# Optimization experiments

Hardware: AMD Instinct MI355X
Metric: run time of the kernel (lower is better)

## Reference

```python
import jax, jax.numpy as jnp
import numpy as np

WS = 7            # window size
NW = 64           # windows per image ((56/7)^2)
SHIFT = 3         # shift size for the SW-MSA mask
HW = 56           # spatial patch grid


def _build_rel_index():
    coords = np.stack(np.meshgrid(np.arange(WS), np.arange(WS), indexing='ij'))  # [2,7,7]
    flat = coords.reshape(2, -1)                                                 # [2,49]
    rel = (flat[:, :, None] - flat[:, None, :]).transpose(1, 2, 0)               # [49,49,2]
    rel[:, :, 0] += WS - 1
    rel[:, :, 1] += WS - 1
    rel[:, :, 0] *= 2 * WS - 1
    return rel.sum(-1).astype(np.int32)                                          # [49,49]


def _build_shift_mask():
    img = np.zeros((HW, HW), dtype=np.float32)
    cnt = 0
    sl = (slice(0, -WS), slice(-WS, -SHIFT), slice(-SHIFT, None))
    for h in sl:
        for w in sl:
            img[h, w] = cnt
            cnt += 1
    # window partition -> [nW, 49]
    mw = img.reshape(HW // WS, WS, HW // WS, WS).transpose(0, 2, 1, 3).reshape(-1, WS * WS)
    am = mw[:, None, :] - mw[:, :, None]                                          # [nW,49,49]
    return np.where(am != 0, -100.0, 0.0).astype(np.float32)


def setup_inputs() -> dict:
    key = jax.random.key(0)
    ks = jax.random.split(key, 6)
    dim, heads, N = 128, 4, WS * WS
    B_ = 4096
    return {
        'x': jax.random.normal(ks[0], (B_, N, dim), dtype=jnp.float32),
        'qkv_w': jax.random.normal(ks[1], (dim, 3 * dim), dtype=jnp.float32) * 0.02,
        'qkv_b': jax.random.normal(ks[2], (3 * dim,), dtype=jnp.float32) * 0.02,
        'proj_w': jax.random.normal(ks[3], (dim, dim), dtype=jnp.float32) * 0.02,
        'proj_b': jax.random.normal(ks[4], (dim,), dtype=jnp.float32) * 0.02,
        'rel_bias_table': jax.random.normal(ks[5], ((2 * WS - 1) ** 2, heads), dtype=jnp.float32) * 0.02,
        'mask': jnp.asarray(_build_shift_mask()),
        'rel_index': jnp.asarray(_build_rel_index()),
    }


def reference(x, qkv_w, qkv_b, proj_w, proj_b, rel_bias_table, mask, rel_index):
    B_, N, C = x.shape
    heads = rel_bias_table.shape[1]
    hd = C // heads
    scale = hd ** -0.5
    # fused qkv projection: [B_, N, 3, H, hd]
    qkv = (x @ qkv_w + qkv_b).reshape(B_, N, 3, heads, hd)
    q, k, v = qkv[:, :, 0], qkv[:, :, 1], qkv[:, :, 2]      # [B_, N, H, hd]
    attn = jnp.einsum('bnhd,bmhd->bhnm', q, k) * scale       # [B_, H, N, N]
    # relative position bias gather: [N,N,H] -> [H,N,N]
    bias = rel_bias_table[rel_index].transpose(2, 0, 1)
    attn = attn + bias[None]
    # shifted-window mask: mask [nW, N, N]
    nW = mask.shape[0]
    attn = attn.reshape(B_ // nW, nW, heads, N, N) + mask[None, :, None]
    attn = attn.reshape(B_, heads, N, N)
    attn = jax.nn.softmax(attn, axis=-1)
    out = jnp.einsum('bhnm,bmhd->bnhd', attn, v).reshape(B_, N, C)
    return out @ proj_w + proj_b
```

## Files before the change

kernel.cpp:

```cpp
#include <hip/hip_runtime.h>
#include <hip/hip_bf16.h>

typedef __attribute__((ext_vector_type(8))) short bf16x8;
typedef __attribute__((ext_vector_type(4))) short s16x4;
typedef __attribute__((ext_vector_type(4))) float f32x4;

#define NTOK 49

#define XROW    136
#define RVB     8704
#define VBT_STR 68
#define VBT_SZ  2176
#define RQK     17408
#define QK_SZ   3920
#define SM_TOT  33088

__device__ __forceinline__ short f2b(float v) {
    __hip_bfloat16 b = __float2bfloat16(v);
    return *reinterpret_cast<short*>(&b);
}

__device__ __forceinline__ int rid_of(int t, int wh, int ww) {
    int i = t / 7;
    int j = t - 7 * i;
    int rh = (wh == 7) ? ((i < 4) ? 1 : 2) : 0;
    int rw = (ww == 7) ? ((j < 4) ? 1 : 2) : 0;
    return rh * 3 + rw;
}

__global__ void prep_kernel(const float* __restrict__ qkv_w,
                            const float* __restrict__ proj_w,
                            const float* __restrict__ rel_tab,
                            const int*   __restrict__ rel_idx,
                            short* __restrict__ wqkv_t,
                            short* __restrict__ wproj_t,
                            float* __restrict__ bmp2) {
    int i = blockIdx.x * 256 + threadIdx.x;
    if (i < 384 * 128) {
        int n = i >> 7, k = i & 127;
        wqkv_t[i] = f2b(qkv_w[k * 384 + n]);
        return;
    }
    int j = i - 384 * 128;
    if (j < 128 * 128) {
        int n = j >> 7, k = j & 127;
        wproj_t[j] = f2b(proj_w[k * 128 + n]);
        return;
    }
    int l = j - 128 * 128;
    if (l < 16 * NTOK * 64) {
        const float LOG2E = 1.4426950408889634f;
        int wt  = l / (4 * NTOK * 64);
        int rem = l - wt * (4 * NTOK * 64);
        int h   = rem / (NTOK * 64);
        int rm2 = rem - h * (NTOK * 64);
        int q = rm2 >> 6, kk = rm2 & 63;
        float v;
        if (kk < NTOK) {
            v = rel_tab[rel_idx[q * NTOK + kk] * 4 + h] * LOG2E;
            int wh = (wt & 1) ? 7 : 0, ww = (wt & 2) ? 7 : 0;
            if (rid_of(q, wh, ww) != rid_of(kk, wh, ww)) v -= 100.0f * LOG2E;
        } else {
            v = -1e30f;
        }
        bmp2[l] = v;
    }
}

__launch_bounds__(512, 4)
__global__ void swin_fused(const float* __restrict__ x,
                           const short* __restrict__ wqkv_t,
                           const float* __restrict__ qkv_b,
                           const short* __restrict__ wproj_t,
                           const float* __restrict__ proj_b,
                           const float* __restrict__ bmp2,
                           float* __restrict__ out) {
    __shared__ short sm[SM_TOT];

    const int b   = blockIdx.x;
    const int tid = threadIdx.x;
    const int wv  = tid >> 6;
    const int ln  = tid & 63;
    const int g   = ln >> 4;
    const int c   = ln & 15;
    const int h    = wv >> 1;
    const int half = wv & 1;

    short* vbt = sm + RVB + h * VBT_SZ;
    short* qbh = sm + RQK + h * QK_SZ;
    short* kbh = qbh + 1960;
    short* pbh = qbh;

    const int cq = 32 * h + 16 * half;

    if (tid < 510) {
        *(s16x4*)&sm[NTOK * XROW + tid * 4] = (s16x4){0, 0, 0, 0};
    }
    for (int idx = tid; idx < 128 * 15; idx += 512) {
        int d = idx / 15, t = 49 + (idx - (idx / 15) * 15);
        sm[RVB + (d >> 5) * VBT_SZ + (d & 31) * VBT_STR + t] = 0;
    }
    {
        const f32x4* xp4 = (const f32x4*)(x + (size_t)b * 6272);
        f32x4 v0 = xp4[tid];
        f32x4 v1 = xp4[tid + 512];
        f32x4 v2 = xp4[tid + 1024];
        f32x4 v3;
        if (tid < 32) v3 = xp4[tid + 1536];
        #define XWR(IDX, V) { int row = (IDX) >> 5; int col = ((IDX) & 31) * 4; \
            s16x4 pk; pk[0]=f2b((V)[0]); pk[1]=f2b((V)[1]); pk[2]=f2b((V)[2]); pk[3]=f2b((V)[3]); \
            *(s16x4*)&sm[row * XROW + col] = pk; }
        XWR(tid, v0) XWR(tid + 512, v1) XWR(tid + 1024, v2)
        if (tid < 32) XWR(tid + 1536, v3)
        #undef XWR
    }
    bf16x8 wqr[4], wkr[4];
    #pragma unroll
    for (int kt = 0; kt < 4; ++kt) {
        wqr[kt] = *(const bf16x8*)&wqkv_t[(cq + c) * 128 + 32*kt + 8*g];
        wkr[kt] = *(const bf16x8*)&wqkv_t[(128 + cq + c) * 128 + 32*kt + 8*g];
    }
    __syncthreads();

    bf16x8 wvr[4];
    {
        f32x4 accq[4], acck[4];
        #pragma unroll
        for (int nt = 0; nt < 4; ++nt) { accq[nt] = (f32x4){0.f,0.f,0.f,0.f}; acck[nt] = (f32x4){0.f,0.f,0.f,0.f}; }
        #pragma unroll
        for (int kt = 0; kt < 4; ++kt) {
            bf16x8 xv[4];
            #pragma unroll
            for (int nt = 0; nt < 4; ++nt)
                xv[nt] = *(const bf16x8*)&sm[(16*nt + c) * XROW + 32*kt + 8*g];
            #pragma unroll
            for (int nt = 0; nt < 4; ++nt) {
                accq[nt] = __builtin_amdgcn_mfma_f32_16x16x32_bf16(wqr[kt], xv[nt], accq[nt], 0, 0, 0);
                acck[nt] = __builtin_amdgcn_mfma_f32_16x16x32_bf16(wkr[kt], xv[nt], acck[nt], 0, 0, 0);
            }
        }
        #pragma unroll
        for (int kt = 0; kt < 4; ++kt)
            wvr[kt] = *(const bf16x8*)&wqkv_t[(256 + cq + c) * 128 + 32*kt + 8*g];

        const float qsc = 0.17677669529663687f * 1.4426950408889634f;
        f32x4 bq4 = *(const f32x4*)&qkv_b[cq + 4*g];
        f32x4 bk4 = *(const f32x4*)&qkv_b[128 + cq + 4*g];
        #pragma unroll
        for (int nt = 0; nt < 4; ++nt) {
            int tok = 16*nt + c;
            if (tok >= NTOK) continue;
            s16x4 pq, pk2;
            #pragma unroll
            for (int r = 0; r < 4; ++r) {
                pq[r]  = f2b((accq[nt][r] + bq4[r]) * qsc);
                pk2[r] = f2b(acck[nt][r] + bk4[r]);
            }
            *(s16x4*)&qbh[tok * 40 + 16*half + 4*g] = pq;
            *(s16x4*)&kbh[tok * 40 + 16*half + 4*g] = pk2;
        }
    }

    {
        f32x4 accv[4];
        #pragma unroll
        for (int nt = 0; nt < 4; ++nt) accv[nt] = (f32x4){0.f,0.f,0.f,0.f};
        #pragma unroll
        for (int kt = 0; kt < 4; ++kt) {
            bf16x8 xv[4];
            #pragma unroll
            for (int nt = 0; nt < 4; ++nt)
                xv[nt] = *(const bf16x8*)&sm[(16*nt + c) * XROW + 32*kt + 8*g];
            #pragma unroll
            for (int nt = 0; nt < 4; ++nt)
                accv[nt] = __builtin_amdgcn_mfma_f32_16x16x32_bf16(wvr[kt], xv[nt], accv[nt], 0, 0, 0);
        }
        f32x4 bv4 = *(const f32x4*)&qkv_b[256 + cq + 4*g];
        const int d0 = 16*half + 4*g;
        #pragma unroll
        for (int nt = 0; nt < 4; ++nt) {
            int tok = 16*nt + c;
            if (tok >= NTOK) continue;
            vbt[(d0+0) * VBT_STR + tok] = f2b(accv[nt][0] + bv4[0]);
            vbt[(d0+1) * VBT_STR + tok] = f2b(accv[nt][1] + bv4[1]);
            vbt[(d0+2) * VBT_STR + tok] = f2b(accv[nt][2] + bv4[2]);
            vbt[(d0+3) * VBT_STR + tok] = f2b(accv[nt][3] + bv4[3]);
        }
    }

    const int ntq0 = 2 * half;
    const int wt = ((((b >> 3) & 7) == 7) ? 1 : 0) | (((b & 7) == 7) ? 2 : 0);
    const float* bbase = bmp2 + ((size_t)(wt * 4 + h) * NTOK) * 64;
    f32x4 bias0[4], bias1[4];
    {
        int q0c = 16*ntq0 + c;       if (q0c > 48) q0c = 48;
        int q1c = 16*(ntq0+1) + c;   if (q1c > 48) q1c = 48;
        const float* bp0 = bbase + (size_t)q0c * 64;
        const float* bp1 = bbase + (size_t)q1c * 64;
        #pragma unroll
        for (int mt = 0; mt < 4; ++mt) {
            bias0[mt] = *(const f32x4*)&bp0[16*mt + 4*g];
            bias1[mt] = *(const f32x4*)&bp1[16*mt + 4*g];
        }
    }
    __syncthreads();

    f32x4 sA[4][2];
    {
        #pragma unroll
        for (int mt = 0; mt < 4; ++mt) { sA[mt][0] = (f32x4){0.f,0.f,0.f,0.f}; sA[mt][1] = (f32x4){0.f,0.f,0.f,0.f}; }
        bf16x8 ak[4];
        #pragma unroll
        for (int mt = 0; mt < 4; ++mt) {
            int kt2 = 16*mt + c; if (kt2 > 48) kt2 = 48;
            ak[mt] = *(const bf16x8*)&kbh[kt2 * 40 + 8*g];
        }
        #pragma unroll
        for (int jj = 0; jj < 2; ++jj) {
            int qt = 16*(ntq0+jj) + c; if (qt > 48) qt = 48;
            bf16x8 bq = *(const bf16x8*)&qbh[qt * 40 + 8*g];
            #pragma unroll
            for (int mt = 0; mt < 4; ++mt)
                sA[mt][jj] = __builtin_amdgcn_mfma_f32_16x16x32_bf16(ak[mt], bq, sA[mt][jj], 0, 0, 0);
        }
    }
    __syncthreads();

    {
        float rs01[2];
        #pragma unroll
        for (int jj = 0; jj < 2; ++jj) {
            int qtok = 16*(ntq0+jj) + c;
            const f32x4* bias = jj ? bias1 : bias0;
            float e[16];
            float mx = -1e30f;
            #pragma unroll
            for (int mt = 0; mt < 4; ++mt) {
                #pragma unroll
                for (int r = 0; r < 4; ++r) {
                    float v = sA[mt][jj][r] + bias[mt][r];
                    e[4*mt+r] = v;
                    mx = fmaxf(mx, v);
                }
            }
            mx = fmaxf(mx, __shfl_xor(mx, 16, 64));
            mx = fmaxf(mx, __shfl_xor(mx, 32, 64));
            float s = 0.f;
            #pragma unroll
            for (int ii = 0; ii < 16; ++ii) { float ev = exp2f(e[ii] - mx); e[ii] = ev; s += ev; }
            if (qtok < NTOK) {
                #pragma unroll
                for (int mt = 0; mt < 4; ++mt) {
                    s16x4 pk;
                    pk[0] = f2b(e[4*mt+0]);
                    pk[1] = f2b(e[4*mt+1]);
                    pk[2] = f2b(e[4*mt+2]);
                    pk[3] = f2b(e[4*mt+3]);
                    *(s16x4*)&pbh[qtok * 72 + 16*mt + 4*g] = pk;
                }
            }
            s += __shfl_xor(s, 16, 64);
            s += __shfl_xor(s, 32, 64);
            rs01[jj] = 1.0f / s;
        }

        f32x4 o[2][2];
        o[0][0]=(f32x4){0.f,0.f,0.f,0.f}; o[0][1]=(f32x4){0.f,0.f,0.f,0.f};
        o[1][0]=(f32x4){0.f,0.f,0.f,0.f}; o[1][1]=(f32x4){0.f,0.f,0.f,0.f};
        #pragma unroll
        for (int kt = 0; kt < 2; ++kt) {
            bf16x8 av[2];
            #pragma unroll
            for (int mt = 0; mt < 2; ++mt)
                av[mt] = *(const bf16x8*)&vbt[(16*mt + c) * VBT_STR + 32*kt + 8*g];
            #pragma unroll
            for (int jj = 0; jj < 2; ++jj) {
                int qt = 16*(ntq0+jj) + c; if (qt > 48) qt = 48;
                bf16x8 bp2 = *(const bf16x8*)&pbh[qt * 72 + 32*kt + 8*g];
                #pragma unroll
                for (int mt = 0; mt < 2; ++mt)
                    o[mt][jj] = __builtin_amdgcn_mfma_f32_16x16x32_bf16(av[mt], bp2, o[mt][jj], 0, 0, 0);
            }
        }
        #pragma unroll
        for (int jj = 0; jj < 2; ++jj) {
            int qtok = 16*(ntq0+jj) + c;
            if (qtok >= NTOK) continue;
            float rs = rs01[jj];
            #pragma unroll
            for (int mt = 0; mt < 2; ++mt) {
                s16x4 pko;
                pko[0] = f2b(o[mt][jj][0] * rs); pko[1] = f2b(o[mt][jj][1] * rs);
                pko[2] = f2b(o[mt][jj][2] * rs); pko[3] = f2b(o[mt][jj][3] * rs);
                *(s16x4*)&pbh[qtok * 72 + 16*mt + 4*g] = pko;
            }
        }
    }
    __syncthreads();

    {
        const int chb = 16 * wv;
        bf16x8 awr[4];
        #pragma unroll
        for (int kt = 0; kt < 4; ++kt)
            awr[kt] = *(const bf16x8*)&wproj_t[(chb + c) * 128 + 32*kt + 8*g];
        f32x4 pb4 = *(const f32x4*)&proj_b[chb + 4*g];
        f32x4 po[4];
        #pragma unroll
        for (int j = 0; j < 4; ++j) po[j] = (f32x4){0.f,0.f,0.f,0.f};
        #pragma unroll
        for (int kt = 0; kt < 4; ++kt) {
            const short* ob_kt = sm + RQK + kt * QK_SZ;
            #pragma unroll
            for (int j = 0; j < 4; ++j) {
                int qt = 16*j + c; if (qt > 48) qt = 48;
                bf16x8 bo = *(const bf16x8*)&ob_kt[qt * 72 + 8*g];
                po[j] = __builtin_amdgcn_mfma_f32_16x16x32_bf16(awr[kt], bo, po[j], 0, 0, 0);
            }
        }
        float* op = out + (size_t)b * 6272;
        #pragma unroll
        for (int j = 0; j < 4; ++j) {
            int qtok = 16*j + c;
            if (qtok >= NTOK) continue;
            f32x4 w;
            w[0] = po[j][0] + pb4[0]; w[1] = po[j][1] + pb4[1];
            w[2] = po[j][2] + pb4[2]; w[3] = po[j][3] + pb4[3];
            *(f32x4*)&op[qtok * 128 + chb + 4*g] = w;
        }
    }
}

extern "C" void kernel_launch(void* const* d_in, const int* in_sizes, int n_in,
                              void* d_out, int out_size, void* d_ws, size_t ws_size,
                              hipStream_t stream) {
    const float* x       = (const float*)d_in[0];
    const float* qkv_w   = (const float*)d_in[1];
    const float* qkv_b   = (const float*)d_in[2];
    const float* proj_w  = (const float*)d_in[3];
    const float* proj_b  = (const float*)d_in[4];
    const float* rel_tab = (const float*)d_in[5];
    const int*   rel_idx = (const int*)d_in[7];

    char* ws = (char*)d_ws;
    short* wqkv_t  = (short*)ws;
    short* wproj_t = (short*)(ws + 98304);
    float* bmp2    = (float*)(ws + 98304 + 32768);

    int total = 384*128 + 128*128 + 16*NTOK*64;
    prep_kernel<<<(total + 255) / 256, 256, 0, stream>>>(qkv_w, proj_w, rel_tab, rel_idx,
                                                         wqkv_t, wproj_t, bmp2);

    int B_ = in_sizes[0] / (NTOK * 128);
    swin_fused<<<B_, 512, 0, stream>>>(x, wqkv_t, qkv_b, wproj_t, proj_b, bmp2,
                                       (float*)d_out);
}
```

Measured before the change: 129.4 us.

## Alias V buffer onto X staging area and cut registers to raise occupancy

The V-transpose buffer now reuses the shared-memory region of the X tile once the QKV projections finish, which shrinks LDS per block. An extra barrier protects the reuse. Weight and bias loads are moved from long-lived register arrays into the loops where they are used, and launch bounds ask for 6 blocks per CU instead of 4. The aim is more resident blocks to hide latency, at the cost of an added sync and global loads that sit on the critical path instead of being prefetched.

```diff
diff --git a/kernel.cpp b/kernel.cpp
--- a/kernel.cpp
+++ b/kernel.cpp
@@ -8,12 +8,11 @@
 #define NTOK 49
 
 #define XROW    136
-#define RVB     8704
 #define VBT_STR 68
 #define VBT_SZ  2176
-#define RQK     17408
+#define RQK     8704
 #define QK_SZ   3920
-#define SM_TOT  33088
+#define SM_TOT  24384
 
 __device__ __forceinline__ short f2b(float v) {
     __hip_bfloat16 b = __float2bfloat16(v);
@@ -67,7 +66,7 @@
     }
 }
 
-__launch_bounds__(512, 4)
+__launch_bounds__(512, 6)
 __global__ void swin_fused(const float* __restrict__ x,
                            const short* __restrict__ wqkv_t,
                            const float* __restrict__ qkv_b,
@@ -86,7 +85,7 @@
     const int h    = wv >> 1;
     const int half = wv & 1;
 
-    short* vbt = sm + RVB + h * VBT_SZ;
+    short* vbt = sm + h * VBT_SZ;
     short* qbh = sm + RQK + h * QK_SZ;
     short* kbh = qbh + 1960;
     short* pbh = qbh;
@@ -95,10 +94,6 @@
 
     if (tid < 510) {
         *(s16x4*)&sm[NTOK * XROW + tid * 4] = (s16x4){0, 0, 0, 0};
-    }
-    for (int idx = tid; idx < 128 * 15; idx += 512) {
-        int d = idx / 15, t = 49 + (idx - (idx / 15) * 15);
-        sm[RVB + (d >> 5) * VBT_SZ + (d & 31) * VBT_STR + t] = 0;
     }
     {
         const f32x4* xp4 = (const f32x4*)(x + (size_t)b * 6272);
@@ -114,35 +109,26 @@
         if (tid < 32) XWR(tid + 1536, v3)
         #undef XWR
     }
-    bf16x8 wqr[4], wkr[4];
-    #pragma unroll
-    for (int kt = 0; kt < 4; ++kt) {
-        wqr[kt] = *(const bf16x8*)&wqkv_t[(cq + c) * 128 + 32*kt + 8*g];
-        wkr[kt] = *(const bf16x8*)&wqkv_t[(128 + cq + c) * 128 + 32*kt + 8*g];
-    }
     __syncthreads();
 
-    bf16x8 wvr[4];
     {
         f32x4 accq[4], acck[4];
         #pragma unroll
         for (int nt = 0; nt < 4; ++nt) { accq[nt] = (f32x4){0.f,0.f,0.f,0.f}; acck[nt] = (f32x4){0.f,0.f,0.f,0.f}; }
         #pragma unroll
         for (int kt = 0; kt < 4; ++kt) {
+            bf16x8 awq = *(const bf16x8*)&wqkv_t[(cq + c) * 128 + 32*kt + 8*g];
+            bf16x8 awk = *(const bf16x8*)&wqkv_t[(128 + cq + c) * 128 + 32*kt + 8*g];
             bf16x8 xv[4];
             #pragma unroll
             for (int nt = 0; nt < 4; ++nt)
                 xv[nt] = *(const bf16x8*)&sm[(16*nt + c) * XROW + 32*kt + 8*g];
             #pragma unroll
             for (int nt = 0; nt < 4; ++nt) {
-                accq[nt] = __builtin_amdgcn_mfma_f32_16x16x32_bf16(wqr[kt], xv[nt], accq[nt], 0, 0, 0);
-                acck[nt] = __builtin_amdgcn_mfma_f32_16x16x32_bf16(wkr[kt], xv[nt], acck[nt], 0, 0, 0);
-            }
-        }
-        #pragma unroll
-        for (int kt = 0; kt < 4; ++kt)
-            wvr[kt] = *(const bf16x8*)&wqkv_t[(256 + cq + c) * 128 + 32*kt + 8*g];
-
+                accq[nt] = __builtin_amdgcn_mfma_f32_16x16x32_bf16(awq, xv[nt], accq[nt], 0, 0, 0);
+                acck[nt] = __builtin_amdgcn_mfma_f32_16x16x32_bf16(awk, xv[nt], acck[nt], 0, 0, 0);
+            }
+        }
         const float qsc = 0.17677669529663687f * 1.4426950408889634f;
         f32x4 bq4 = *(const f32x4*)&qkv_b[cq + 4*g];
         f32x4 bk4 = *(const f32x4*)&qkv_b[128 + cq + 4*g];
@@ -167,13 +153,19 @@
         for (int nt = 0; nt < 4; ++nt) accv[nt] = (f32x4){0.f,0.f,0.f,0.f};
         #pragma unroll
         for (int kt = 0; kt < 4; ++kt) {
+            bf16x8 awv = *(const bf16x8*)&wqkv_t[(256 + cq + c) * 128 + 32*kt + 8*g];
             bf16x8 xv[4];
             #pragma unroll
             for (int nt = 0; nt < 4; ++nt)
                 xv[nt] = *(const bf16x8*)&sm[(16*nt + c) * XROW + 32*kt + 8*g];
             #pragma unroll
             for (int nt = 0; nt < 4; ++nt)
-                accv[nt] = __builtin_amdgcn_mfma_f32_16x16x32_bf16(wvr[kt], xv[nt], accv[nt], 0, 0, 0);
+                accv[nt] = __builtin_amdgcn_mfma_f32_16x16x32_bf16(awv, xv[nt], accv[nt], 0, 0, 0);
+        }
+        __syncthreads();
+        for (int idx = tid; idx < 128 * 15; idx += 512) {
+            int d = idx / 15, t = 49 + (idx - (idx / 15) * 15);
+            sm[(d >> 5) * VBT_SZ + (d & 31) * VBT_STR + t] = 0;
         }
         f32x4 bv4 = *(const f32x4*)&qkv_b[256 + cq + 4*g];
         const int d0 = 16*half + 4*g;
@@ -187,24 +179,9 @@
             vbt[(d0+3) * VBT_STR + tok] = f2b(accv[nt][3] + bv4[3]);
         }
     }
+    __syncthreads();
 
     const int ntq0 = 2 * half;
-    const int wt = ((((b >> 3) & 7) == 7) ? 1 : 0) | (((b & 7) == 7) ? 2 : 0);
-    const float* bbase = bmp2 + ((size_t)(wt * 4 + h) * NTOK) * 64;
-    f32x4 bias0[4], bias1[4];
-    {
-        int q0c = 16*ntq0 + c;       if (q0c > 48) q0c = 48;
-        int q1c = 16*(ntq0+1) + c;   if (q1c > 48) q1c = 48;
-        const float* bp0 = bbase + (size_t)q0c * 64;
-        const float* bp1 = bbase + (size_t)q1c * 64;
-        #pragma unroll
-        for (int mt = 0; mt < 4; ++mt) {
-            bias0[mt] = *(const f32x4*)&bp0[16*mt + 4*g];
-            bias1[mt] = *(const f32x4*)&bp1[16*mt + 4*g];
-        }
-    }
-    __syncthreads();
-
     f32x4 sA[4][2];
     {
         #pragma unroll
@@ -227,18 +204,22 @@
     __syncthreads();
 
     {
+        const int wt = ((((b >> 3) & 7) == 7) ? 1 : 0) | (((b & 7) == 7) ? 2 : 0);
+        const float* bbase = bmp2 + ((size_t)(wt * 4 + h) * NTOK) * 64;
         float rs01[2];
         #pragma unroll
         for (int jj = 0; jj < 2; ++jj) {
             int qtok = 16*(ntq0+jj) + c;
-            const f32x4* bias = jj ? bias1 : bias0;
+            int qtokc = qtok > 48 ? 48 : qtok;
+            const float* bp = bbase + (size_t)qtokc * 64;
             float e[16];
             float mx = -1e30f;
             #pragma unroll
             for (int mt = 0; mt < 4; ++mt) {
+                f32x4 b4 = *(const f32x4*)&bp[16*mt + 4*g];
                 #pragma unroll
                 for (int r = 0; r < 4; ++r) {
-                    float v = sA[mt][jj][r] + bias[mt][r];
+                    float v = sA[mt][jj][r] + b4[r];
                     e[4*mt+r] = v;
                     mx = fmaxf(mx, v);
                 }
@@ -300,24 +281,21 @@
 
     {
         const int chb = 16 * wv;
-        bf16x8 awr[4];
-        #pragma unroll
-        for (int kt = 0; kt < 4; ++kt)
-            awr[kt] = *(const bf16x8*)&wproj_t[(chb + c) * 128 + 32*kt + 8*g];
-        f32x4 pb4 = *(const f32x4*)&proj_b[chb + 4*g];
         f32x4 po[4];
         #pragma unroll
         for (int j = 0; j < 4; ++j) po[j] = (f32x4){0.f,0.f,0.f,0.f};
         #pragma unroll
         for (int kt = 0; kt < 4; ++kt) {
+            bf16x8 aw = *(const bf16x8*)&wproj_t[(chb + c) * 128 + 32*kt + 8*g];
             const short* ob_kt = sm + RQK + kt * QK_SZ;
             #pragma unroll
             for (int j = 0; j < 4; ++j) {
                 int qt = 16*j + c; if (qt > 48) qt = 48;
                 bf16x8 bo = *(const bf16x8*)&ob_kt[qt * 72 + 8*g];
-                po[j] = __builtin_amdgcn_mfma_f32_16x16x32_bf16(awr[kt], bo, po[j], 0, 0, 0);
-            }
-        }
+                po[j] = __builtin_amdgcn_mfma_f32_16x16x32_bf16(aw, bo, po[j], 0, 0, 0);
+            }
+        }
+        f32x4 pb4 = *(const f32x4*)&proj_b[chb + 4*g];
         float* op = out + (size_t)b * 6272;
         #pragma unroll
         for (int j = 0; j < 4; ++j) {
```

New measurement: 161.9 us. 1.25x slower.
